# Kernel optimization log

Measured on AMD Instinct MI355X. Metric: run time of the kernel, lower is better.

The kernel has to match this reference:

```python
import jax, jax.numpy as jnp
import numpy as np

DIM = 384; HEADS = 6; K = 10; G = 2
GC = DIM // G            # group channel dim
HD = DIM // HEADS        # head dim
SCALE = HD ** -0.5
LN_EPS = 1e-5


def _sqdist(a, b):
    # a: [..., n, 3], b: [..., m, 3] -> [..., n, m]
    return (jnp.sum(a * a, -1)[..., :, None]
            + jnp.sum(b * b, -1)[..., None, :]
            - 2.0 * jnp.einsum('...nc,...mc->...nm', a, b))


def setup_inputs() -> dict:
    key = jax.random.key(0)
    ks = jax.random.split(key, 12)
    B, N, M = 4, 1024, 1024
    s = 0.02
    return {
        'q': jax.random.normal(ks[0], (B, N, DIM), jnp.float32),
        'q_pos': jax.random.normal(ks[1], (B, N, 3), jnp.float32),
        'v': jax.random.normal(ks[2], (B, M, DIM), jnp.float32),
        'v_pos': jax.random.normal(ks[3], (B, M, 3), jnp.float32),
        'Wq': jax.random.normal(ks[4], (DIM, DIM), jnp.float32) * s,
        'Wk': jax.random.normal(ks[5], (DIM, DIM), jnp.float32) * s,
        'Wv': jax.random.normal(ks[6], (DIM, DIM), jnp.float32) * s,
        'Wvoff': jax.random.normal(ks[7], (DIM, DIM), jnp.float32) * s,
        'Woff1': jax.random.normal(ks[8], (DIM, 2 * GC), jnp.float32) * s,
        'boff1': jnp.zeros((DIM,), jnp.float32),
        'ln_g': jnp.ones((DIM,), jnp.float32),
        'ln_b': jnp.zeros((DIM,), jnp.float32),
        'Woff2': jax.random.normal(ks[9], (3, DIM), jnp.float32) * s,
        'Wproj': jax.random.normal(ks[10], (DIM, DIM), jnp.float32) * s,
        'bproj': jnp.zeros((DIM,), jnp.float32),
    }


def reference(q, q_pos, v, v_pos, Wq, Wk, Wv, Wvoff, Woff1, boff1,
              ln_g, ln_b, Woff2, Wproj, bproj):
    B, N, C = q.shape
    M = v.shape[1]

    # --- knn_point: K nearest v_pos for each q_pos ---
    idx = jax.lax.top_k(-_sqdist(q_pos, v_pos), K)[1]        # [B,N,K]
    idx_flat = idx.reshape(B, N * K, 1)

    qp = q @ Wq.T                                            # [B,N,C]
    v_off = v @ Wvoff.T                                      # [B,M,C]

    # index_points gathers
    local_v = jnp.take_along_axis(v_off, idx_flat, axis=1).reshape(B, N, K, C)
    local_v_pos = jnp.take_along_axis(v_pos, idx_flat, axis=1).reshape(B, N, K, 3)

    # group split: 'b n k (g c) -> b g n k c'
    off_local_v = local_v.reshape(B, N, K, G, GC).transpose(0, 3, 1, 2, 4)  # [B,G,N,K,GC]
    group_q = qp.reshape(B, N, G, GC).transpose(0, 2, 1, 3)                 # [B,G,N,GC]

    shift_feat = jnp.concatenate(
        [off_local_v, jnp.broadcast_to(group_q[:, :, :, None, :], (B, G, N, K, GC))], -1)

    # linear_offset MLP: Linear -> LayerNorm -> GELU(exact) -> Linear, then tanh
    h = shift_feat @ Woff1.T + boff1                          # [B,G,N,K,DIM]
    mu = h.mean(-1, keepdims=True)
    var = h.var(-1, keepdims=True)
    h = (h - mu) / jnp.sqrt(var + LN_EPS) * ln_g + ln_b
    h = jax.nn.gelu(h, approximate=False)
    offset = jnp.tanh(h @ Woff2.T)                            # [B,G,N,K,3]

    shift_pos = (local_v_pos[:, None] + offset).reshape(B, G, N * K, 3)
    vg = v.reshape(B, M, G, GC).transpose(0, 2, 1, 3)         # [B,G,M,GC]

    # --- three_nn + reciprocal-distance three_interpolate ---
    sqd = _sqdist(shift_pos, v_pos[:, None])                  # [B,G,N*K,M]
    negd, idx3 = jax.lax.top_k(-sqd, 3)                       # 3 smallest
    dist = jnp.sqrt(jnp.maximum(-negd, 0.0))                  # [B,G,N*K,3]
    w = 1.0 / (dist + 1e-8)
    w = w / jnp.sum(w, -1, keepdims=True)
    feats = jnp.take_along_axis(vg, idx3.reshape(B, G, N * K * 3, 1), axis=2)
    feats = feats.reshape(B, G, N * K, 3, GC)
    interp = jnp.einsum('bgnj,bgnjc->bgnc', w, feats)         # [B,G,N*K,GC]
    # '(b g) (n k) c -> b n k (g c)'
    interp = interp.reshape(B, G, N, K, GC).transpose(0, 2, 3, 1, 4).reshape(B, N, K, C)

    # --- local cross-attention (each query attends to its K interpolated feats) ---
    kf = (interp @ Wk.T).reshape(B, N, K, HEADS, HD)
    vf = (interp @ Wv.T).reshape(B, N, K, HEADS, HD)
    qh = qp.reshape(B, N, HEADS, HD)
    attn = jnp.einsum('bnhd,bnkhd->bhnk', qh, kf) * SCALE
    attn = jax.nn.softmax(attn, axis=-1)
    out = jnp.einsum('bhnk,bnkhd->bnhd', attn, vf).reshape(B, N, C)
    return out @ Wproj.T + bproj
```

## Files before the change

kernel.cpp:

```cpp
#include <hip/hip_runtime.h>
#include <math.h>

#define NB 4
#define NN 1024
#define NM 1024
#define NC 384
#define NK 10
#define NG 2
#define NGC 192
#define NH 6

#define GSZ ((size_t)NB * NM * NC)

#define OFF_WQ 0
#define OFF_W1B 147456
#define OFF_WK0 221184
#define OFF_WK1 294912
#define OFF_WV0 368640
#define OFF_WV1 442368
#define OFF_WPROJ 516096
#define WT_ALL_FLOATS 663552

__device__ __forceinline__ float wred_sum(float v) {
#pragma unroll
  for (int m = 32; m >= 1; m >>= 1) v += __shfl_xor(v, m, 64);
  return v;
}

__device__ __forceinline__ void wred_argmin(float& d, int& m) {
#pragma unroll
  for (int off = 32; off >= 1; off >>= 1) {
    float od = __shfl_xor(d, off, 64);
    int om = __shfl_xor(m, off, 64);
    if (od < d || (od == d && om < m)) { d = od; m = om; }
  }
}

__global__ void transpose_all_k(const float* __restrict__ Wq, const float* __restrict__ Woff1,
                                const float* __restrict__ Wk, const float* __restrict__ Wv,
                                const float* __restrict__ Wproj, float* __restrict__ Wt_all) {
  const float* W;
  int i0, icount, doff;
  switch (blockIdx.y) {
    case 0: W = Wq;    i0 = 0;   icount = NC;  doff = OFF_WQ;    break;
    case 1: W = Woff1; i0 = NGC; icount = NGC; doff = OFF_W1B;   break;
    case 2: W = Wk;    i0 = 0;   icount = NGC; doff = OFF_WK0;   break;
    case 3: W = Wk;    i0 = NGC; icount = NGC; doff = OFF_WK1;   break;
    case 4: W = Wv;    i0 = 0;   icount = NGC; doff = OFF_WV0;   break;
    case 5: W = Wv;    i0 = NGC; icount = NGC; doff = OFF_WV1;   break;
    default: W = Wproj; i0 = 0;  icount = NC;  doff = OFF_WPROJ; break;
  }
  int id = blockIdx.x * 256 + threadIdx.x;
  if (id >= icount * NC) return;
  int o = id % NC;
  int i = id / NC;
  Wt_all[doff + (size_t)i * NC + o] = W[(size_t)o * NC + i0 + i];
}

__global__ void wcomb_k(const float* __restrict__ Woff1, const float* __restrict__ Wvoff,
                        float* __restrict__ Wcomb_t) {
  int o = blockIdx.x;
  int g = blockIdx.y;
  int i = threadIdx.x;
  __shared__ float w1[NGC];
  if (i < NGC) w1[i] = Woff1[(size_t)o * NC + i];
  __syncthreads();
  float acc = 0.f;
#pragma unroll 4
  for (int j = 0; j < NGC; ++j)
    acc = fmaf(w1[j], Wvoff[(size_t)(g * NGC + j) * NC + i], acc);
  Wcomb_t[((size_t)g * NC + i) * NC + o] = acc;
}

__global__ __launch_bounds__(384) void gemm16_k(const float* __restrict__ X, int IN, int xoff0,
                                                int xoff_stride, const float* __restrict__ Wt0,
                                                size_t wstride, const float* __restrict__ bias,
                                                float* __restrict__ Y0, size_t ystride) {
  __shared__ __align__(16) float xs[NC][20];
  int tid = threadIdx.x;
  int og = tid % 96, rg = tid / 96;
  int r0 = blockIdx.x * 16;
  int job = blockIdx.y;
  int xoff = xoff0 + job * xoff_stride;
  const float* Wt = Wt0 + (size_t)job * wstride;
  float* Y = Y0 + (size_t)job * ystride;
  for (int t = tid; t < 16 * IN; t += 384) {
    int r = t / IN, kk = t % IN;
    xs[kk][r] = X[(size_t)(r0 + r) * NC + xoff + kk];
  }
  __syncthreads();
  float acc[4][4];
#pragma unroll
  for (int i = 0; i < 4; ++i)
#pragma unroll
    for (int j = 0; j < 4; ++j) acc[i][j] = 0.f;
  int o = og * 4;
#pragma unroll 4
  for (int kk = 0; kk < IN; ++kk) {
    float4 w4 = *(const float4*)&Wt[(size_t)kk * NC + o];
    float4 x4 = *(const float4*)&xs[kk][rg * 4];
    float xr[4] = {x4.x, x4.y, x4.z, x4.w};
    float wr[4] = {w4.x, w4.y, w4.z, w4.w};
#pragma unroll
    for (int ri = 0; ri < 4; ++ri)
#pragma unroll
      for (int oi = 0; oi < 4; ++oi) acc[ri][oi] = fmaf(xr[ri], wr[oi], acc[ri][oi]);
  }
  float4 bv = make_float4(0.f, 0.f, 0.f, 0.f);
  if (bias) bv = *(const float4*)&bias[o];
#pragma unroll
  for (int ri = 0; ri < 4; ++ri) {
    float4 ov;
    ov.x = acc[ri][0] + bv.x;
    ov.y = acc[ri][1] + bv.y;
    ov.z = acc[ri][2] + bv.z;
    ov.w = acc[ri][3] + bv.w;
    *(float4*)&Y[(size_t)(r0 + rg * 4 + ri) * NC + o] = ov;
  }
}

__global__ __launch_bounds__(384) void vproj_k(const float* __restrict__ v,
                                               const float* __restrict__ Wcomb_t,
                                               const float* __restrict__ Wt_all,
                                               float* __restrict__ vcontrib,
                                               float* __restrict__ KcT,
                                               float* __restrict__ VcT) {
  __shared__ __align__(16) float xs[NC][20];
  int tid = threadIdx.x;
  int og = tid % 96, rg = tid / 96;
  int r0 = blockIdx.x * 16;
  int job = blockIdx.y;
  const float* Wt;
  float* Y;
  int IN, xoff;
  switch (job) {
    case 0: Wt = Wcomb_t;                 Y = vcontrib;       IN = NC;  xoff = 0;   break;
    case 1: Wt = Wcomb_t + (size_t)NC * NC; Y = vcontrib + GSZ; IN = NC;  xoff = 0;   break;
    case 2: Wt = Wt_all + OFF_WK0;        Y = KcT;            IN = NGC; xoff = 0;   break;
    case 3: Wt = Wt_all + OFF_WK1;        Y = KcT + GSZ;      IN = NGC; xoff = NGC; break;
    case 4: Wt = Wt_all + OFF_WV0;        Y = VcT;            IN = NGC; xoff = 0;   break;
    default: Wt = Wt_all + OFF_WV1;       Y = VcT + GSZ;      IN = NGC; xoff = NGC; break;
  }
  for (int t = tid; t < 16 * IN; t += 384) {
    int r = t / IN, kk = t % IN;
    xs[kk][r] = v[(size_t)(r0 + r) * NC + xoff + kk];
  }
  __syncthreads();
  float acc[4][4];
#pragma unroll
  for (int i = 0; i < 4; ++i)
#pragma unroll
    for (int j = 0; j < 4; ++j) acc[i][j] = 0.f;
  int o = og * 4;
#pragma unroll 4
  for (int kk = 0; kk < IN; ++kk) {
    float4 w4 = *(const float4*)&Wt[(size_t)kk * NC + o];
    float4 x4 = *(const float4*)&xs[kk][rg * 4];
    float xr[4] = {x4.x, x4.y, x4.z, x4.w};
    float wr[4] = {w4.x, w4.y, w4.z, w4.w};
#pragma unroll
    for (int ri = 0; ri < 4; ++ri)
#pragma unroll
      for (int oi = 0; oi < 4; ++oi) acc[ri][oi] = fmaf(xr[ri], wr[oi], acc[ri][oi]);
  }
#pragma unroll
  for (int ri = 0; ri < 4; ++ri)
    *(float4*)&Y[(size_t)(r0 + rg * 4 + ri) * NC + o] =
        make_float4(acc[ri][0], acc[ri][1], acc[ri][2], acc[ri][3]);
}

__global__ __launch_bounds__(256) void knn2_k(const float* __restrict__ q_pos,
                                              const float* __restrict__ v_pos,
                                              int* __restrict__ knn_idx) {
  __shared__ float px[NM], py[NM], pz[NM], ss[NM];
  int tid = threadIdx.x, lane = tid & 63, wid = tid >> 6;
  int b = blockIdx.x / (NN / 4);
  int n = (blockIdx.x % (NN / 4)) * 4 + wid;
  for (int t = tid; t < NM; t += 256) {
    float x = v_pos[((size_t)b * NM + t) * 3 + 0];
    float y = v_pos[((size_t)b * NM + t) * 3 + 1];
    float z = v_pos[((size_t)b * NM + t) * 3 + 2];
    px[t] = x; py[t] = y; pz[t] = z;
    ss[t] = x * x + y * y + z * z;
  }
  __syncthreads();
  float qx = q_pos[((size_t)b * NN + n) * 3 + 0];
  float qy = q_pos[((size_t)b * NN + n) * 3 + 1];
  float qz = q_pos[((size_t)b * NN + n) * 3 + 2];
  float qq = qx * qx + qy * qy + qz * qz;
  float bd[NK];
  int bi[NK];
#pragma unroll
  for (int j = 0; j < NK; ++j) { bd[j] = 1e30f; bi[j] = 0x7fffffff; }
#pragma unroll
  for (int t = 0; t < NM / 64; ++t) {
    int m = t * 64 + lane;
    float d = qq + ss[m] - 2.f * (qx * px[m] + qy * py[m] + qz * pz[m]);
    if (d < bd[NK - 1]) {
#pragma unroll
      for (int j = NK - 1; j > 0; --j) {
        if (d < bd[j - 1]) { bd[j] = bd[j - 1]; bi[j] = bi[j - 1]; }
        else if (d < bd[j]) { bd[j] = d; bi[j] = m; }
      }
      if (d < bd[0]) { bd[0] = d; bi[0] = m; }
    }
  }
  size_t base = ((size_t)b * NN + n) * NK;
#pragma unroll
  for (int round = 0; round < NK; ++round) {
    float dh = bd[0];
    int mh = bi[0];
    wred_argmin(dh, mh);
    if (lane == 0) knn_idx[base + round] = mh;
    if (bi[0] == mh) {
#pragma unroll
      for (int j = 0; j < NK - 1; ++j) { bd[j] = bd[j + 1]; bi[j] = bi[j + 1]; }
      bd[NK - 1] = 1e30f; bi[NK - 1] = 0x7fffffff;
    }
  }
}

__global__ __launch_bounds__(256) void mlp3nn_k(
    const float* __restrict__ vcontrib, const float* __restrict__ qcontrib,
    const float* __restrict__ boff1, const float* __restrict__ ln_g,
    const float* __restrict__ ln_b, const float* __restrict__ Woff2,
    const int* __restrict__ knn_idx, const float* __restrict__ v_pos,
    int* __restrict__ idx3, float* __restrict__ w3) {
  __shared__ float px[NM], py[NM], pz[NM], ss[NM];
  int tid = threadIdx.x, lane = tid & 63, wid = tid >> 6;
  int r = blockIdx.x * 4 + wid;
  int b = (blockIdx.x * 4) / (NK * NN * NG);
  for (int t = tid; t < NM; t += 256) {
    float x = v_pos[((size_t)b * NM + t) * 3 + 0];
    float y = v_pos[((size_t)b * NM + t) * 3 + 1];
    float z = v_pos[((size_t)b * NM + t) * 3 + 2];
    px[t] = x; py[t] = y; pz[t] = z;
    ss[t] = x * x + y * y + z * z;
  }
  __syncthreads();
  int k = r % NK;
  int n = (r / NK) % NN;
  int g = (r / (NK * NN)) % NG;
  int m = knn_idx[((size_t)b * NN + n) * NK + k];
  const float* vc = vcontrib + ((size_t)(g * NB + b) * NM + m) * NC;
  const float* qc = qcontrib + ((size_t)(g * NB + b) * NN + n) * NC;
  float h[6];
  float s = 0.f, s2 = 0.f;
#pragma unroll
  for (int j = 0; j < 6; ++j) {
    int c = j * 64 + lane;
    float x = vc[c] + qc[c] + boff1[c];
    h[j] = x; s += x; s2 += x * x;
  }
  s = wred_sum(s);
  s2 = wred_sum(s2);
  float mean = s * (1.f / NC);
  float var = s2 * (1.f / NC) - mean * mean;
  float inv = 1.f / sqrtf(var + 1e-5f);
  float p0 = 0.f, p1 = 0.f, p2 = 0.f;
#pragma unroll
  for (int j = 0; j < 6; ++j) {
    int c = j * 64 + lane;
    float x = (h[j] - mean) * inv * ln_g[c] + ln_b[c];
    x = 0.5f * x * (1.f + erff(x * 0.70710678118654752f));
    p0 = fmaf(x, Woff2[0 * NC + c], p0);
    p1 = fmaf(x, Woff2[1 * NC + c], p1);
    p2 = fmaf(x, Woff2[2 * NC + c], p2);
  }
  p0 = wred_sum(p0);
  p1 = wred_sum(p1);
  p2 = wred_sum(p2);
  float sx = px[m] + tanhf(p0);
  float sy = py[m] + tanhf(p1);
  float sz = pz[m] + tanhf(p2);
  float qq2 = sx * sx + sy * sy + sz * sz;
  float d0v = 1e30f, d1v = 1e30f, d2v = 1e30f;
  int i0v = 0x7fffffff, i1v = 0x7fffffff, i2v = 0x7fffffff;
#pragma unroll
  for (int t = 0; t < NM / 64; ++t) {
    int m2 = t * 64 + lane;
    float d = qq2 + ss[m2] - 2.f * (sx * px[m2] + sy * py[m2] + sz * pz[m2]);
    if (d < d2v) {
      d2v = d; i2v = m2;
      if (d2v < d1v) { float td = d1v; d1v = d2v; d2v = td; int ti = i1v; i1v = i2v; i2v = ti; }
      if (d1v < d0v) { float td = d0v; d0v = d1v; d1v = td; int ti = i0v; i0v = i1v; i1v = ti; }
    }
  }
  float rd[3];
  int rm[3];
#pragma unroll
  for (int round = 0; round < 3; ++round) {
    float dh = d0v;
    int mh = i0v;
    wred_argmin(dh, mh);
    rd[round] = dh; rm[round] = mh;
    if (i0v == mh) {
      d0v = d1v; i0v = i1v;
      d1v = d2v; i1v = i2v;
      d2v = 1e30f; i2v = 0x7fffffff;
    }
  }
  if (lane == 0) {
    float e0 = 1.f / (sqrtf(fmaxf(rd[0], 0.f)) + 1e-8f);
    float e1 = 1.f / (sqrtf(fmaxf(rd[1], 0.f)) + 1e-8f);
    float e2 = 1.f / (sqrtf(fmaxf(rd[2], 0.f)) + 1e-8f);
    float sw = e0 + e1 + e2;
    idx3[(size_t)r * 3 + 0] = rm[0]; w3[(size_t)r * 3 + 0] = e0 / sw;
    idx3[(size_t)r * 3 + 1] = rm[1]; w3[(size_t)r * 3 + 1] = e1 / sw;
    idx3[(size_t)r * 3 + 2] = rm[2]; w3[(size_t)r * 3 + 2] = e2 / sw;
  }
}

__global__ __launch_bounds__(NC) void attn_k(const float* __restrict__ qp,
                                             const float* __restrict__ Kc,
                                             const float* __restrict__ Vc,
                                             const int* __restrict__ idx3,
                                             const float* __restrict__ w3,
                                             float* __restrict__ attn_out) {
  __shared__ float vfs[NK][NC];
  __shared__ float lgs[NH][NK];
  __shared__ int il[NG][NK][3];
  __shared__ float wl[NG][NK][3];
  int o = threadIdx.x;
  int lane = o & 63, wid = o >> 6;
  int b = blockIdx.x / NN;
  int n = blockIdx.x % NN;
  if (o < NG * NK * 3) {
    int g = o / (NK * 3), k = (o / 3) % NK, j = o % 3;
    size_t rr = (((size_t)(b * NG + g) * NN + n) * NK + k) * 3 + j;
    il[g][k][j] = idx3[rr];
    wl[g][k][j] = w3[rr];
  }
  __syncthreads();
  float qv = qp[((size_t)b * NN + n) * NC + o];
  for (int k = 0; k < NK; ++k) {
    float kf = 0.f, vf = 0.f;
#pragma unroll
    for (int g = 0; g < NG; ++g)
#pragma unroll
      for (int j = 0; j < 3; ++j) {
        int m = il[g][k][j];
        float w = wl[g][k][j];
        size_t base = ((size_t)(g * NB + b) * NM + m) * NC + o;
        kf = fmaf(w, Kc[base], kf);
        vf = fmaf(w, Vc[base], vf);
      }
    vfs[k][o] = vf;
    float p = wred_sum(qv * kf);
    if (lane == 0) lgs[wid][k] = p * 0.125f;
  }
  __syncthreads();
  float a[NK];
  float mx = -1e30f;
#pragma unroll
  for (int k = 0; k < NK; ++k) { a[k] = lgs[wid][k]; mx = fmaxf(mx, a[k]); }
  float sum = 0.f;
#pragma unroll
  for (int k = 0; k < NK; ++k) { a[k] = expf(a[k] - mx); sum += a[k]; }
  float outv = 0.f;
#pragma unroll
  for (int k = 0; k < NK; ++k) outv = fmaf(a[k] / sum, vfs[k][o], outv);
  attn_out[((size_t)b * NN + n) * NC + o] = outv;
}

extern "C" void kernel_launch(void* const* d_in, const int* in_sizes, int n_in,
                              void* d_out, int out_size, void* d_ws, size_t ws_size,
                              hipStream_t stream) {
  (void)in_sizes; (void)n_in; (void)out_size; (void)ws_size;
  const float* q     = (const float*)d_in[0];
  const float* q_pos = (const float*)d_in[1];
  const float* v     = (const float*)d_in[2];
  const float* v_pos = (const float*)d_in[3];
  const float* Wq    = (const float*)d_in[4];
  const float* Wk    = (const float*)d_in[5];
  const float* Wv    = (const float*)d_in[6];
  const float* Wvoff = (const float*)d_in[7];
  const float* Woff1 = (const float*)d_in[8];
  const float* boff1 = (const float*)d_in[9];
  const float* ln_g  = (const float*)d_in[10];
  const float* ln_b  = (const float*)d_in[11];
  const float* Woff2 = (const float*)d_in[12];
  const float* Wproj = (const float*)d_in[13];
  const float* bproj = (const float*)d_in[14];
  float* out = (float*)d_out;

  char* p = (char*)d_ws;
  auto alloc_f = [&](size_t n) { float* r = (float*)p; p += n * sizeof(float); return r; };
  auto alloc_i = [&](size_t n) { int* r = (int*)p; p += n * sizeof(int); return r; };

  float* qp        = alloc_f((size_t)NB * NN * NC);
  float* qcontrib  = alloc_f((size_t)NG * NB * NN * NC);
  float* vcontrib  = alloc_f((size_t)NG * NB * NM * NC);
  float* KcT       = alloc_f((size_t)NG * NB * NM * NC);
  float* VcT       = alloc_f((size_t)NG * NB * NM * NC);
  float* Wt_all    = alloc_f((size_t)WT_ALL_FLOATS);
  float* Wcomb_t   = alloc_f((size_t)NG * NC * NC);
  float* w3        = alloc_f((size_t)NB * NG * NN * NK * 3);
  int* knn_idx     = alloc_i((size_t)NB * NN * NK);
  int* idx3        = alloc_i((size_t)NB * NG * NN * NK * 3);
  float* attn_out  = vcontrib;

  transpose_all_k<<<dim3(576, 7), 256, 0, stream>>>(Wq, Woff1, Wk, Wv, Wproj, Wt_all);
  wcomb_k<<<dim3(NC, NG), NC, 0, stream>>>(Woff1, Wvoff, Wcomb_t);

  gemm16_k<<<dim3(NB * NN / 16, 1), 384, 0, stream>>>(q, NC, 0, 0, Wt_all + OFF_WQ, 0, nullptr,
                                                      qp, 0);
  knn2_k<<<NB * (NN / 4), 256, 0, stream>>>(q_pos, v_pos, knn_idx);
  gemm16_k<<<dim3(NB * NN / 16, 2), 384, 0, stream>>>(qp, NGC, 0, NGC, Wt_all + OFF_W1B, 0,
                                                      nullptr, qcontrib, (size_t)NB * NN * NC);
  vproj_k<<<dim3(NB * NM / 16, 6), 384, 0, stream>>>(v, Wcomb_t, Wt_all, vcontrib, KcT, VcT);

  mlp3nn_k<<<NB * NG * NN * NK / 4, 256, 0, stream>>>(vcontrib, qcontrib, boff1, ln_g, ln_b,
                                                      Woff2, knn_idx, v_pos, idx3, w3);
  attn_k<<<NB * NN, NC, 0, stream>>>(qp, KcT, VcT, idx3, w3, attn_out);
  gemm16_k<<<dim3(NB * NN / 16, 1), 384, 0, stream>>>(attn_out, NC, 0, 0, Wt_all + OFF_WPROJ, 0,
                                                      bproj, out, 0);
}
```

Before: 475.0 us.

## Fold Wq into offset weights, merge projection GEMMs, store K/V in bf16

Precomputes combined weights Woff1·Wq for the query contribution so qcontrib comes directly from q, and merges the q projection, qcontrib and v projections into a single 9-job kernel launch. The per-point K and V projection outputs are stored as bf16, halving the gather traffic in the attention kernel. The knn and 3-NN kernels pack positions and squared norms into a float4 shared array so each candidate takes one LDS load. The bf16 storage loses precision in K/V features, and the weight folding changes the floating-point summation order.

Measured after the change: 497.7 us. 4.8% more time.

```diff
diff --git a/kernel.cpp b/kernel.cpp
--- a/kernel.cpp
+++ b/kernel.cpp
@@ -11,6 +11,8 @@
 #define NH 6
 
 #define GSZ ((size_t)NB * NM * NC)
+#define QSZ ((size_t)NB * NN * NC)
+#define NCNC ((size_t)NC * NC)
 
 #define OFF_WQ 0
 #define OFF_W1B 147456
@@ -34,6 +36,15 @@
     int om = __shfl_xor(m, off, 64);
     if (od < d || (od == d && om < m)) { d = od; m = om; }
   }
+}
+
+__device__ __forceinline__ ushort f2bf(float x) {
+  unsigned u = __float_as_uint(x);
+  unsigned r = (u + 0x7fffu + ((u >> 16) & 1u)) >> 16;
+  return (ushort)r;
+}
+__device__ __forceinline__ float b2f(ushort s) {
+  return __uint_as_float(((unsigned)s) << 16);
 }
 
 __global__ void transpose_all_k(const float* __restrict__ Wq, const float* __restrict__ Woff1,
@@ -57,19 +68,24 @@
   Wt_all[doff + (size_t)i * NC + o] = W[(size_t)o * NC + i0 + i];
 }
 
-__global__ void wcomb_k(const float* __restrict__ Woff1, const float* __restrict__ Wvoff,
-                        float* __restrict__ Wcomb_t) {
+__global__ __launch_bounds__(256) void wcomb2_k(const float* __restrict__ Woff1,
+                                                const float* __restrict__ Wvoff,
+                                                const float* __restrict__ Wq,
+                                                float* __restrict__ WcombAll) {
   int o = blockIdx.x;
-  int g = blockIdx.y;
-  int i = threadIdx.x;
+  int job = blockIdx.y;
+  int g = job & 1, kind = job >> 1;
+  const float* Wsrc = kind ? Wq : Wvoff;
   __shared__ float w1[NGC];
-  if (i < NGC) w1[i] = Woff1[(size_t)o * NC + i];
-  __syncthreads();
-  float acc = 0.f;
+  for (int j = threadIdx.x; j < NGC; j += 256) w1[j] = Woff1[(size_t)o * NC + kind * NGC + j];
+  __syncthreads();
+  for (int i = threadIdx.x; i < NC; i += 256) {
+    float acc = 0.f;
 #pragma unroll 4
-  for (int j = 0; j < NGC; ++j)
-    acc = fmaf(w1[j], Wvoff[(size_t)(g * NGC + j) * NC + i], acc);
-  Wcomb_t[((size_t)g * NC + i) * NC + o] = acc;
+    for (int j = 0; j < NGC; ++j)
+      acc = fmaf(w1[j], Wsrc[(size_t)(g * NGC + j) * NC + i], acc);
+    WcombAll[((size_t)job * NC + i) * NC + o] = acc;
+  }
 }
 
 __global__ __launch_bounds__(384) void gemm16_k(const float* __restrict__ X, int IN, int xoff0,
@@ -119,31 +135,39 @@
   }
 }
 
-__global__ __launch_bounds__(384) void vproj_k(const float* __restrict__ v,
-                                               const float* __restrict__ Wcomb_t,
-                                               const float* __restrict__ Wt_all,
-                                               float* __restrict__ vcontrib,
-                                               float* __restrict__ KcT,
-                                               float* __restrict__ VcT) {
+__global__ __launch_bounds__(384) void projall_k(const float* __restrict__ q,
+                                                 const float* __restrict__ v,
+                                                 const float* __restrict__ WcombAll,
+                                                 const float* __restrict__ Wt_all,
+                                                 float* __restrict__ qp,
+                                                 float* __restrict__ qcontrib,
+                                                 float* __restrict__ vcontrib,
+                                                 ushort* __restrict__ KcT,
+                                                 ushort* __restrict__ VcT) {
   __shared__ __align__(16) float xs[NC][20];
   int tid = threadIdx.x;
   int og = tid % 96, rg = tid / 96;
   int r0 = blockIdx.x * 16;
   int job = blockIdx.y;
+  const float* X;
   const float* Wt;
-  float* Y;
   int IN, xoff;
+  float* Yf = nullptr;
+  ushort* Yh = nullptr;
   switch (job) {
-    case 0: Wt = Wcomb_t;                 Y = vcontrib;       IN = NC;  xoff = 0;   break;
-    case 1: Wt = Wcomb_t + (size_t)NC * NC; Y = vcontrib + GSZ; IN = NC;  xoff = 0;   break;
-    case 2: Wt = Wt_all + OFF_WK0;        Y = KcT;            IN = NGC; xoff = 0;   break;
-    case 3: Wt = Wt_all + OFF_WK1;        Y = KcT + GSZ;      IN = NGC; xoff = NGC; break;
-    case 4: Wt = Wt_all + OFF_WV0;        Y = VcT;            IN = NGC; xoff = 0;   break;
-    default: Wt = Wt_all + OFF_WV1;       Y = VcT + GSZ;      IN = NGC; xoff = NGC; break;
+    case 0: X = v; IN = NC;  xoff = 0;   Wt = WcombAll;            Yf = vcontrib;       break;
+    case 1: X = v; IN = NC;  xoff = 0;   Wt = WcombAll + NCNC;     Yf = vcontrib + GSZ; break;
+    case 2: X = v; IN = NGC; xoff = 0;   Wt = Wt_all + OFF_WK0;    Yh = KcT;            break;
+    case 3: X = v; IN = NGC; xoff = NGC; Wt = Wt_all + OFF_WK1;    Yh = KcT + GSZ;      break;
+    case 4: X = v; IN = NGC; xoff = 0;   Wt = Wt_all + OFF_WV0;    Yh = VcT;            break;
+    case 5: X = v; IN = NGC; xoff = NGC; Wt = Wt_all + OFF_WV1;    Yh = VcT + GSZ;      break;
+    case 6: X = q; IN = NC;  xoff = 0;   Wt = Wt_all + OFF_WQ;     Yf = qp;             break;
+    case 7: X = q; IN = NC;  xoff = 0;   Wt = WcombAll + 2 * NCNC; Yf = qcontrib;       break;
+    default:X = q; IN = NC;  xoff = 0;   Wt = WcombAll + 3 * NCNC; Yf = qcontrib + QSZ; break;
   }
   for (int t = tid; t < 16 * IN; t += 384) {
     int r = t / IN, kk = t % IN;
-    xs[kk][r] = v[(size_t)(r0 + r) * NC + xoff + kk];
+    xs[kk][r] = X[(size_t)(r0 + r) * NC + xoff + kk];
   }
   __syncthreads();
   float acc[4][4];
@@ -163,16 +187,28 @@
 #pragma unroll
       for (int oi = 0; oi < 4; ++oi) acc[ri][oi] = fmaf(xr[ri], wr[oi], acc[ri][oi]);
   }
-#pragma unroll
-  for (int ri = 0; ri < 4; ++ri)
-    *(float4*)&Y[(size_t)(r0 + rg * 4 + ri) * NC + o] =
-        make_float4(acc[ri][0], acc[ri][1], acc[ri][2], acc[ri][3]);
+  if (Yf) {
+#pragma unroll
+    for (int ri = 0; ri < 4; ++ri)
+      *(float4*)&Yf[(size_t)(r0 + rg * 4 + ri) * NC + o] =
+          make_float4(acc[ri][0], acc[ri][1], acc[ri][2], acc[ri][3]);
+  } else {
+#pragma unroll
+    for (int ri = 0; ri < 4; ++ri) {
+      ushort4 pk;
+      pk.x = f2bf(acc[ri][0]);
+      pk.y = f2bf(acc[ri][1]);
+      pk.z = f2bf(acc[ri][2]);
+      pk.w = f2bf(acc[ri][3]);
+      *(ushort4*)&Yh[(size_t)(r0 + rg * 4 + ri) * NC + o] = pk;
+    }
+  }
 }
 
 __global__ __launch_bounds__(256) void knn2_k(const float* __restrict__ q_pos,
                                               const float* __restrict__ v_pos,
                                               int* __restrict__ knn_idx) {
-  __shared__ float px[NM], py[NM], pz[NM], ss[NM];
+  __shared__ float4 cpos[NM];
   int tid = threadIdx.x, lane = tid & 63, wid = tid >> 6;
   int b = blockIdx.x / (NN / 4);
   int n = (blockIdx.x % (NN / 4)) * 4 + wid;
@@ -180,8 +216,7 @@
     float x = v_pos[((size_t)b * NM + t) * 3 + 0];
     float y = v_pos[((size_t)b * NM + t) * 3 + 1];
     float z = v_pos[((size_t)b * NM + t) * 3 + 2];
-    px[t] = x; py[t] = y; pz[t] = z;
-    ss[t] = x * x + y * y + z * z;
+    cpos[t] = make_float4(x, y, z, x * x + y * y + z * z);
   }
   __syncthreads();
   float qx = q_pos[((size_t)b * NN + n) * 3 + 0];
@@ -195,7 +230,8 @@
 #pragma unroll
   for (int t = 0; t < NM / 64; ++t) {
     int m = t * 64 + lane;
-    float d = qq + ss[m] - 2.f * (qx * px[m] + qy * py[m] + qz * pz[m]);
+    float4 cc = cpos[m];
+    float d = qq + cc.w - 2.f * (qx * cc.x + qy * cc.y + qz * cc.z);
     if (d < bd[NK - 1]) {
 #pragma unroll
       for (int j = NK - 1; j > 0; --j) {
@@ -226,7 +262,7 @@
     const float* __restrict__ ln_b, const float* __restrict__ Woff2,
     const int* __restrict__ knn_idx, const float* __restrict__ v_pos,
     int* __restrict__ idx3, float* __restrict__ w3) {
-  __shared__ float px[NM], py[NM], pz[NM], ss[NM];
+  __shared__ float4 cpos[NM];
   int tid = threadIdx.x, lane = tid & 63, wid = tid >> 6;
   int r = blockIdx.x * 4 + wid;
   int b = (blockIdx.x * 4) / (NK * NN * NG);
@@ -234,8 +270,7 @@
     float x = v_pos[((size_t)b * NM + t) * 3 + 0];
     float y = v_pos[((size_t)b * NM + t) * 3 + 1];
     float z = v_pos[((size_t)b * NM + t) * 3 + 2];
-    px[t] = x; py[t] = y; pz[t] = z;
-    ss[t] = x * x + y * y + z * z;
+    cpos[t] = make_float4(x, y, z, x * x + y * y + z * z);
   }
   __syncthreads();
   int k = r % NK;
@@ -270,16 +305,18 @@
   p0 = wred_sum(p0);
   p1 = wred_sum(p1);
   p2 = wred_sum(p2);
-  float sx = px[m] + tanhf(p0);
-  float sy = py[m] + tanhf(p1);
-  float sz = pz[m] + tanhf(p2);
+  float4 cm = cpos[m];
+  float sx = cm.x + tanhf(p0);
+  float sy = cm.y + tanhf(p1);
+  float sz = cm.z + tanhf(p2);
   float qq2 = sx * sx + sy * sy + sz * sz;
   float d0v = 1e30f, d1v = 1e30f, d2v = 1e30f;
   int i0v = 0x7fffffff, i1v = 0x7fffffff, i2v = 0x7fffffff;
 #pragma unroll
   for (int t = 0; t < NM / 64; ++t) {
     int m2 = t * 64 + lane;
-    float d = qq2 + ss[m2] - 2.f * (sx * px[m2] + sy * py[m2] + sz * pz[m2]);
+    float4 cc = cpos[m2];
+    float d = qq2 + cc.w - 2.f * (sx * cc.x + sy * cc.y + sz * cc.z);
     if (d < d2v) {
       d2v = d; i2v = m2;
       if (d2v < d1v) { float td = d1v; d1v = d2v; d2v = td; int ti = i1v; i1v = i2v; i2v = ti; }
@@ -312,8 +349,8 @@
 }
 
 __global__ __launch_bounds__(NC) void attn_k(const float* __restrict__ qp,
-                                             const float* __restrict__ Kc,
-                                             const float* __restrict__ Vc,
+                                             const ushort* __restrict__ Kc,
+                                             const ushort* __restrict__ Vc,
                                              const int* __restrict__ idx3,
                                              const float* __restrict__ w3,
                                              float* __restrict__ attn_out) {
@@ -342,8 +379,8 @@
         int m = il[g][k][j];
         float w = wl[g][k][j];
         size_t base = ((size_t)(g * NB + b) * NM + m) * NC + o;
-        kf = fmaf(w, Kc[base], kf);
-        vf = fmaf(w, Vc[base], vf);
+        kf = fmaf(w, b2f(Kc[base]), kf);
+        vf = fmaf(w, b2f(Vc[base]), vf);
       }
     vfs[k][o] = vf;
     float p = wred_sum(qv * kf);
@@ -386,29 +423,27 @@
 
   char* p = (char*)d_ws;
   auto alloc_f = [&](size_t n) { float* r = (float*)p; p += n * sizeof(float); return r; };
+  auto alloc_h = [&](size_t n) { ushort* r = (ushort*)p; p += n * sizeof(ushort); return r; };
   auto alloc_i = [&](size_t n) { int* r = (int*)p; p += n * sizeof(int); return r; };
 
-  float* qp        = alloc_f((size_t)NB * NN * NC);
-  float* qcontrib  = alloc_f((size_t)NG * NB * NN * NC);
-  float* vcontrib  = alloc_f((size_t)NG * NB * NM * NC);
-  float* KcT       = alloc_f((size_t)NG * NB * NM * NC);
-  float* VcT       = alloc_f((size_t)NG * NB * NM * NC);
+  float* qp        = alloc_f(QSZ);
+  float* qcontrib  = alloc_f((size_t)NG * QSZ);
+  float* vcontrib  = alloc_f((size_t)NG * GSZ);
   float* Wt_all    = alloc_f((size_t)WT_ALL_FLOATS);
-  float* Wcomb_t   = alloc_f((size_t)NG * NC * NC);
+  float* WcombAll  = alloc_f((size_t)4 * NCNC);
   float* w3        = alloc_f((size_t)NB * NG * NN * NK * 3);
+  ushort* KcT      = alloc_h((size_t)NG * GSZ);
+  ushort* VcT      = alloc_h((size_t)NG * GSZ);
   int* knn_idx     = alloc_i((size_t)NB * NN * NK);
   int* idx3        = alloc_i((size_t)NB * NG * NN * NK * 3);
   float* attn_out  = vcontrib;
 
   transpose_all_k<<<dim3(576, 7), 256, 0, stream>>>(Wq, Woff1, Wk, Wv, Wproj, Wt_all);
-  wcomb_k<<<dim3(NC, NG), NC, 0, stream>>>(Woff1, Wvoff, Wcomb_t);
-
-  gemm16_k<<<dim3(NB * NN / 16, 1), 384, 0, stream>>>(q, NC, 0, 0, Wt_all + OFF_WQ, 0, nullptr,
-                                                      qp, 0);
+  wcomb2_k<<<dim3(NC, 4), 256, 0, stream>>>(Woff1, Wvoff, Wq, WcombAll);
   knn2_k<<<NB * (NN / 4), 256, 0, stream>>>(q_pos, v_pos, knn_idx);
-  gemm16_k<<<dim3(NB * NN / 16, 2), 384, 0, stream>>>(qp, NGC, 0, NGC, Wt_all + OFF_W1B, 0,
-                                                      nullptr, qcontrib, (size_t)NB * NN * NC);
-  vproj_k<<<dim3(NB * NM / 16, 6), 384, 0, stream>>>(v, Wcomb_t, Wt_all, vcontrib, KcT, VcT);
+
+  projall_k<<<dim3(NB * NM / 16, 9), 384, 0, stream>>>(q, v, WcombAll, Wt_all, qp, qcontrib,
+                                                       vcontrib, KcT, VcT);
 
   mlp3nn_k<<<NB * NG * NN * NK / 4, 256, 0, stream>>>(vcontrib, qcontrib, boff1, ln_g, ln_b,
                                                       Woff2, knn_idx, v_pos, idx3, w3);
```
